# Kernel optimization log

Hardware: AMD Instinct MI355X
Metric: run time of the kernel (lower is better)

The kernel has to match this reference:

```python
import jax, jax.numpy as jnp
import numpy as np


def setup_inputs() -> dict:
    key = jax.random.key(0)
    k1, k2, k3 = jax.random.split(key, 3)
    B, S, IN, OUT = 4, 2048, 4096, 4096
    # int8 activations, weights, bias (stored as int8; math accumulates in int32)
    x = jax.random.randint(k1, (B, S, IN), -127, 128, dtype=jnp.int32).astype(jnp.int8)
    weight = jax.random.randint(k2, (OUT, IN), -127, 128, dtype=jnp.int32).astype(jnp.int8)  # (out, in)
    bias = jax.random.randint(k3, (1, OUT), -127, 128, dtype=jnp.int32).astype(jnp.int8)
    alpha = jnp.float32(0.001)  # input_scale*weight_scale/output_scale
    beta = jnp.float32(0.01)    # bias_scale/output_scale
    return {"x": x, "weight": weight, "bias": bias, "alpha": alpha, "beta": beta}


def reference(x, weight, bias, alpha, beta):
    # Flatten leading dims: (B,S,IN) -> (N,IN)
    x_shape = x.shape
    xf = x.reshape(-1, x_shape[-1])
    acc = jax.lax.dot_general(
        xf, weight,
        dimension_numbers=(((1,), (1,)), ((), ())),
        preferred_element_type=jnp.int32,
    )  # (N, OUT) int32
    # Fused epilogue: y = round(alpha*acc + beta*bias), saturate to int8
    yf = alpha * acc.astype(jnp.float32) + beta * bias.astype(jnp.float32)
    y = jnp.clip(jnp.round(yf), -128.0, 127.0).astype(jnp.int8)
    return y.reshape(*x_shape[:-1], -1)
```

## Files before the change

### kernel.cpp

```cpp
#include <hip/hip_runtime.h>
#include <stdint.h>

using i32x4  = __attribute__((ext_vector_type(4)))  int;
using i32x16 = __attribute__((ext_vector_type(16))) int;

#define M_TOT 8192
#define N_TOT 4096
#define K_TOT 4096
#define BM 256
#define BN 256

__device__ __forceinline__ void gload_lds16(const void* g, void* l) {
  __builtin_amdgcn_global_load_lds(
      (const __attribute__((address_space(1))) void*)(uintptr_t)g,
      (__attribute__((address_space(3))) void*)(uint32_t)(uintptr_t)l,
      16, 0, 0);
}

__global__ void pack_tiles(const int* __restrict__ a32, const int* __restrict__ b32,
                           int8_t* __restrict__ ap, int8_t* __restrict__ bp,
                           int na, int ntot) {
  int stride = gridDim.x * blockDim.x;
  for (int idx = blockIdx.x * blockDim.x + threadIdx.x; idx < ntot; idx += stride) {
    int i = idx;
    const int* src;
    int8_t* dst;
    if (idx < na) { src = a32; dst = ap; }
    else          { src = b32; dst = bp; i = idx - na; }
    int sp = i & 3;
    int rr = (i >> 2) & 255;
    int kc = (i >> 10) & 63;
    int p  = i >> 16;
    int sl = sp ^ ((rr >> 1) & 3);
    const i32x4* s = (const i32x4*)(src + (((size_t)(p * 256 + rr)) << 12) + kc * 64 + sl * 16);
    i32x4 a = s[0], b = s[1], c = s[2], d = s[3];
    i32x4 o;
    o.x = (a.x & 255) | ((a.y & 255) << 8) | ((a.z & 255) << 16) | (a.w << 24);
    o.y = (b.x & 255) | ((b.y & 255) << 8) | ((b.z & 255) << 16) | (b.w << 24);
    o.z = (c.x & 255) | ((c.y & 255) << 8) | ((c.z & 255) << 16) | (c.w << 24);
    o.w = (d.x & 255) | ((d.y & 255) << 8) | ((d.z & 255) << 16) | (d.w << 24);
    ((i32x4*)dst)[i] = o;
  }
}

#define STAGE_A(KC) {                                                       \
    const int8_t* _g = Asrc + (size_t)(KC) * 16384 + stoff;                 \
    char* _d = lds + ((KC) % 3) * 16384 + stoff;                            \
    gload_lds16(_g, _d); gload_lds16(_g + 8192, _d + 8192); }
#define STAGE_B(KC) {                                                       \
    const int8_t* _g = Bsrc + (size_t)(KC) * 16384 + stoff;                 \
    char* _d = lds + 49152 + ((KC) % 3) * 16384 + stoff;                    \
    gload_lds16(_g, _d); gload_lds16(_g + 8192, _d + 8192); }

#define KTILE(RING, KC2, VM, DO_STAGE) {                                    \
    asm volatile("s_waitcnt vmcnt(" VM ")" ::: "memory");                   \
    __builtin_amdgcn_s_barrier();                                           \
    __builtin_amdgcn_sched_barrier(0);                                      \
    const char* _La = lds + (RING) * 16384;                                 \
    const char* _Lb = lds + 49152 + (RING) * 16384;                         \
    i32x4 A0[2][2], A1[2][2], B0[2][2];                                     \
    _Pragma("unroll") for (int mi = 0; mi < 2; ++mi)                        \
    _Pragma("unroll") for (int ks = 0; ks < 2; ++ks)                        \
      A0[mi][ks] = *(const i32x4*)(_La + aRow[mi] + kOff[ks]);              \
    _Pragma("unroll") for (int ni = 0; ni < 2; ++ni)                        \
    _Pragma("unroll") for (int ks = 0; ks < 2; ++ks)                        \
      B0[ni][ks] = *(const i32x4*)(_Lb + bRow[ni] + kOff[ks]);              \
    if (DO_STAGE) STAGE_A(KC2)                                              \
    __builtin_amdgcn_s_barrier();                                           \
    asm volatile("s_waitcnt lgkmcnt(0)" ::: "memory");                      \
    __builtin_amdgcn_sched_barrier(0);                                      \
    __builtin_amdgcn_s_setprio(1);                                          \
    _Pragma("unroll") for (int ks = 0; ks < 2; ++ks)                        \
    _Pragma("unroll") for (int mi = 0; mi < 2; ++mi)                        \
    _Pragma("unroll") for (int ni = 0; ni < 2; ++ni)                        \
      acc[mi][ni] = __builtin_amdgcn_mfma_i32_32x32x32_i8(A0[mi][ks], B0[ni][ks], acc[mi][ni], 0, 0, 0); \
    __builtin_amdgcn_s_setprio(0);                                          \
    __builtin_amdgcn_s_barrier();                                           \
    _Pragma("unroll") for (int mi = 0; mi < 2; ++mi)                        \
    _Pragma("unroll") for (int ks = 0; ks < 2; ++ks)                        \
      A1[mi][ks] = *(const i32x4*)(_La + aRow[mi + 2] + kOff[ks]);          \
    if (DO_STAGE) STAGE_B(KC2)                                              \
    __builtin_amdgcn_s_barrier();                                           \
    asm volatile("s_waitcnt lgkmcnt(0)" ::: "memory");                      \
    __builtin_amdgcn_sched_barrier(0);                                      \
    __builtin_amdgcn_s_setprio(1);                                          \
    _Pragma("unroll") for (int ks = 0; ks < 2; ++ks)                        \
    _Pragma("unroll") for (int mi = 0; mi < 2; ++mi)                        \
    _Pragma("unroll") for (int ni = 0; ni < 2; ++ni)                        \
      acc[mi + 2][ni] = __builtin_amdgcn_mfma_i32_32x32x32_i8(A1[mi][ks], B0[ni][ks], acc[mi + 2][ni], 0, 0, 0); \
    __builtin_amdgcn_s_setprio(0);                                          \
  }

__global__ __launch_bounds__(512, 2) void gemm_w8a8(
    const int8_t* __restrict__ Apack,
    const int8_t* __restrict__ Bpack,
    const int*    __restrict__ bias,
    const float*  __restrict__ alphap,
    const float*  __restrict__ betap,
    int* __restrict__ out)
{
  __shared__ __align__(16) char lds[98304];

  const int bid = blockIdx.x;
  const int xcd = bid & 7, wi = bid >> 3;
  const int tm = (xcd & 3) * 8 + (wi & 7);
  const int tn = (xcd >> 2) * 8 + (wi >> 3);

  const int tid = threadIdx.x;
  const int w   = tid >> 6;
  const int l   = tid & 63;
  const int lr  = l & 31;
  const int hi  = l >> 5;
  const int wr  = w >> 2;
  const int wc  = w & 3;
  const int stoff = tid * 16;

  const int8_t* Asrc = Apack + ((size_t)tm << 20);
  const int8_t* Bsrc = Bpack + ((size_t)tn << 20);

  const int swz = (lr >> 1) & 3;
  int aRow[4], bRow[2], kOff[2];
#pragma unroll
  for (int mi = 0; mi < 4; ++mi) aRow[mi] = (wr * 128 + mi * 32 + lr) * 64;
#pragma unroll
  for (int ni = 0; ni < 2; ++ni) bRow[ni] = (wc * 64 + ni * 32 + lr) * 64;
#pragma unroll
  for (int ks = 0; ks < 2; ++ks) kOff[ks] = ((((ks << 1) | hi)) ^ swz) * 16;

  i32x16 acc[4][2] = {};

  STAGE_A(0) STAGE_B(0)
  STAGE_A(1) STAGE_B(1)

  for (int t = 0; t < 20; ++t) {
    const int k = t * 3;
    KTILE(0, k + 2, "4", 1)
    KTILE(1, k + 3, "4", 1)
    KTILE(2, k + 4, "4", 1)
  }
  KTILE(0, 62, "4", 1)
  KTILE(1, 63, "4", 1)
  KTILE(2, 0,  "4", 0)
  KTILE(0, 0,  "0", 0)

  const float alpha = *alphap;
  const float beta  = *betap;
  const int brow = tm * BM, bcol = tn * BN;
#pragma unroll
  for (int ni = 0; ni < 2; ++ni) {
    const int col = bcol + wc * 64 + ni * 32 + lr;
    const float bb = beta * (float)bias[col];
#pragma unroll
    for (int mi = 0; mi < 4; ++mi) {
      const int rbase = brow + wr * 128 + mi * 32 + 4 * hi;
#pragma unroll
      for (int r = 0; r < 16; ++r) {
        const int row = rbase + (r & 3) + 8 * (r >> 2);
        float v = alpha * (float)acc[mi][ni][r] + bb;
        v = rintf(v);
        v = fminf(127.f, fmaxf(-128.f, v));
        out[(size_t)row * N_TOT + col] = (int)v;
      }
    }
  }
}

extern "C" void kernel_launch(void* const* d_in, const int* in_sizes, int n_in,
                              void* d_out, int out_size, void* d_ws, size_t ws_size,
                              hipStream_t stream) {
  const int*   x32    = (const int*)d_in[0];
  const int*   w32    = (const int*)d_in[1];
  const int*   bias   = (const int*)d_in[2];
  const float* alphap = (const float*)d_in[3];
  const float* betap  = (const float*)d_in[4];
  int* out = (int*)d_out;

  int8_t* xp = (int8_t*)d_ws;
  int8_t* wp = xp + (size_t)M_TOT * K_TOT;

  const int na   = (M_TOT * K_TOT) / 16;
  const int ntot = na + (N_TOT * K_TOT) / 16;
  pack_tiles<<<3072, 256, 0, stream>>>(x32, w32, xp, wp, na, ntot);

  gemm_w8a8<<<512, 512, 0, stream>>>(xp, wp, bias, alphap, betap, out);
}
```

Before: 203.4 us.

## Switch to double-buffered LDS with register-fragment rotation across K tiles

Changes the LDS ring from three slots to two, dropping shared memory from 96KB to 64KB. The kernel now rotates three register fragment sets so the next tile's first k-slice is read from LDS while the current MFMAs run. Each K tile now uses one barrier and one full vmcnt(0) wait instead of several barriers per tile. The risk is that waiting on vmcnt(0) exposes global load latency, since only one tile of prefetch is in flight, and the extra fragment registers add register pressure.

```diff
diff --git a/kernel.cpp b/kernel.cpp
--- a/kernel.cpp
+++ b/kernel.cpp
@@ -43,53 +43,45 @@
   }
 }
 
-#define STAGE_A(KC) {                                                       \
+#define STAGE_A(KC, SLOT) {                                                 \
     const int8_t* _g = Asrc + (size_t)(KC) * 16384 + stoff;                 \
-    char* _d = lds + ((KC) % 3) * 16384 + stoff;                            \
+    char* _d = lds + (SLOT) * 16384 + stoff;                                \
     gload_lds16(_g, _d); gload_lds16(_g + 8192, _d + 8192); }
-#define STAGE_B(KC) {                                                       \
+#define STAGE_B(KC, SLOT) {                                                 \
     const int8_t* _g = Bsrc + (size_t)(KC) * 16384 + stoff;                 \
-    char* _d = lds + 49152 + ((KC) % 3) * 16384 + stoff;                    \
+    char* _d = lds + 32768 + (SLOT) * 16384 + stoff;                        \
     gload_lds16(_g, _d); gload_lds16(_g + 8192, _d + 8192); }
 
-#define KTILE(RING, KC2, VM, DO_STAGE) {                                    \
-    asm volatile("s_waitcnt vmcnt(" VM ")" ::: "memory");                   \
+#define LOAD_SET(FA, FB, SLOT, KS) {                                        \
+    const char* _pa = lds + (SLOT) * 16384 + kOff[KS];                      \
+    const char* _pb = _pa + 32768;                                          \
+    FA[0] = *(const i32x4*)(_pa + aRow[0]);                                 \
+    FA[1] = *(const i32x4*)(_pa + aRow[1]);                                 \
+    FA[2] = *(const i32x4*)(_pa + aRow[2]);                                 \
+    FA[3] = *(const i32x4*)(_pa + aRow[3]);                                 \
+    FB[0] = *(const i32x4*)(_pb + bRow[0]);                                 \
+    FB[1] = *(const i32x4*)(_pb + bRow[1]); }
+
+#define MFMA8(FA, FB)                                                       \
+    _Pragma("unroll")                                                       \
+    for (int mi = 0; mi < 4; ++mi)                                          \
+    _Pragma("unroll")                                                       \
+    for (int ni = 0; ni < 2; ++ni)                                          \
+      acc[mi][ni] = __builtin_amdgcn_mfma_i32_32x32x32_i8(FA[mi], FB[ni], acc[mi][ni], 0, 0, 0);
+
+#define KTILE(SA_, SB_, SC_, SLOT, KC2, DO_STAGE, DO_NEXT) {                \
+    LOAD_SET(fA##SB_, fB##SB_, SLOT, 1)                                     \
+    asm volatile("s_waitcnt vmcnt(0)" ::: "memory");                        \
     __builtin_amdgcn_s_barrier();                                           \
     __builtin_amdgcn_sched_barrier(0);                                      \
-    const char* _La = lds + (RING) * 16384;                                 \
-    const char* _Lb = lds + 49152 + (RING) * 16384;                         \
-    i32x4 A0[2][2], A1[2][2], B0[2][2];                                     \
-    _Pragma("unroll") for (int mi = 0; mi < 2; ++mi)                        \
-    _Pragma("unroll") for (int ks = 0; ks < 2; ++ks)                        \
-      A0[mi][ks] = *(const i32x4*)(_La + aRow[mi] + kOff[ks]);              \
-    _Pragma("unroll") for (int ni = 0; ni < 2; ++ni)                        \
-    _Pragma("unroll") for (int ks = 0; ks < 2; ++ks)                        \
-      B0[ni][ks] = *(const i32x4*)(_Lb + bRow[ni] + kOff[ks]);              \
-    if (DO_STAGE) STAGE_A(KC2)                                              \
-    __builtin_amdgcn_s_barrier();                                           \
-    asm volatile("s_waitcnt lgkmcnt(0)" ::: "memory");                      \
-    __builtin_amdgcn_sched_barrier(0);                                      \
+    if (DO_STAGE) { STAGE_A(KC2, SLOT) STAGE_B(KC2, SLOT) }                 \
     __builtin_amdgcn_s_setprio(1);                                          \
-    _Pragma("unroll") for (int ks = 0; ks < 2; ++ks)                        \
-    _Pragma("unroll") for (int mi = 0; mi < 2; ++mi)                        \
-    _Pragma("unroll") for (int ni = 0; ni < 2; ++ni)                        \
-      acc[mi][ni] = __builtin_amdgcn_mfma_i32_32x32x32_i8(A0[mi][ks], B0[ni][ks], acc[mi][ni], 0, 0, 0); \
+    MFMA8(fA##SA_, fB##SA_)                                                 \
     __builtin_amdgcn_s_setprio(0);                                          \
-    __builtin_amdgcn_s_barrier();                                           \
-    _Pragma("unroll") for (int mi = 0; mi < 2; ++mi)                        \
-    _Pragma("unroll") for (int ks = 0; ks < 2; ++ks)                        \
-      A1[mi][ks] = *(const i32x4*)(_La + aRow[mi + 2] + kOff[ks]);          \
-    if (DO_STAGE) STAGE_B(KC2)                                              \
-    __builtin_amdgcn_s_barrier();                                           \
-    asm volatile("s_waitcnt lgkmcnt(0)" ::: "memory");                      \
-    __builtin_amdgcn_sched_barrier(0);                                      \
+    if (DO_NEXT) LOAD_SET(fA##SC_, fB##SC_, (SLOT) ^ 1, 0)                  \
     __builtin_amdgcn_s_setprio(1);                                          \
-    _Pragma("unroll") for (int ks = 0; ks < 2; ++ks)                        \
-    _Pragma("unroll") for (int mi = 0; mi < 2; ++mi)                        \
-    _Pragma("unroll") for (int ni = 0; ni < 2; ++ni)                        \
-      acc[mi + 2][ni] = __builtin_amdgcn_mfma_i32_32x32x32_i8(A1[mi][ks], B0[ni][ks], acc[mi + 2][ni], 0, 0, 0); \
-    __builtin_amdgcn_s_setprio(0);                                          \
-  }
+    MFMA8(fA##SB_, fB##SB_)                                                 \
+    __builtin_amdgcn_s_setprio(0); }
 
 __global__ __launch_bounds__(512, 2) void gemm_w8a8(
     const int8_t* __restrict__ Apack,
@@ -99,7 +91,7 @@
     const float*  __restrict__ betap,
     int* __restrict__ out)
 {
-  __shared__ __align__(16) char lds[98304];
+  __shared__ __align__(16) char lds[65536];
 
   const int bid = blockIdx.x;
   const int xcd = bid & 7, wi = bid >> 3;
@@ -128,20 +120,28 @@
   for (int ks = 0; ks < 2; ++ks) kOff[ks] = ((((ks << 1) | hi)) ^ swz) * 16;
 
   i32x16 acc[4][2] = {};
+  i32x4 fA0[4], fB0[2], fA1[4], fB1[2], fA2[4], fB2[2];
 
-  STAGE_A(0) STAGE_B(0)
-  STAGE_A(1) STAGE_B(1)
+  STAGE_A(0, 0) STAGE_B(0, 0)
+  STAGE_A(1, 1) STAGE_B(1, 1)
+  asm volatile("s_waitcnt vmcnt(4)" ::: "memory");
+  __builtin_amdgcn_s_barrier();
+  __builtin_amdgcn_sched_barrier(0);
+  LOAD_SET(fA0, fB0, 0, 0)
 
-  for (int t = 0; t < 20; ++t) {
-    const int k = t * 3;
-    KTILE(0, k + 2, "4", 1)
-    KTILE(1, k + 3, "4", 1)
-    KTILE(2, k + 4, "4", 1)
+  for (int t = 0; t < 10; ++t) {
+    const int kk = t * 6;
+    KTILE(0, 1, 2, 0, kk + 2, 1, 1)
+    KTILE(2, 0, 1, 1, kk + 3, 1, 1)
+    KTILE(1, 2, 0, 0, kk + 4, 1, 1)
+    KTILE(0, 1, 2, 1, kk + 5, 1, 1)
+    KTILE(2, 0, 1, 0, kk + 6, 1, 1)
+    KTILE(1, 2, 0, 1, kk + 7, 1, 1)
   }
-  KTILE(0, 62, "4", 1)
-  KTILE(1, 63, "4", 1)
-  KTILE(2, 0,  "4", 0)
-  KTILE(0, 0,  "0", 0)
+  KTILE(0, 1, 2, 0, 62, 1, 1)
+  KTILE(2, 0, 1, 1, 63, 1, 1)
+  KTILE(1, 2, 0, 0, 0,  0, 1)
+  KTILE(0, 1, 2, 1, 0,  0, 0)
 
   const float alpha = *alphap;
   const float beta  = *betap;
```

Result: faster. 197.5 us (-2.9%).
